# Performance work log

Measured on AMD Instinct MI355X. Metric: run time of the kernel, lower is better.

The kernel has to match this reference:

```python
import jax, jax.numpy as jnp
import numpy as np

D_MODEL = 1024
NUM_HEADS = 16
HEAD_DIM = D_MODEL // NUM_HEADS
THETA = 10000.0
B, S = 4, 2048


def _rope(x, pos):
    # x: [B, H, S, d], pos: [B, S] int
    half = HEAD_DIM // 2
    inv_freq = THETA ** (-(jnp.arange(half, dtype=jnp.float32) * 2.0) / HEAD_DIM)  # [half]
    ang = pos.astype(jnp.float32)[:, None, :, None] * inv_freq  # [B, 1, S, half]
    cos, sin = jnp.cos(ang), jnp.sin(ang)
    x1, x2 = x[..., 0::2], x[..., 1::2]  # interleaved pairs
    r1 = x1 * cos - x2 * sin
    r2 = x1 * sin + x2 * cos
    return jnp.stack([r1, r2], axis=-1).reshape(x.shape)


def setup_inputs() -> dict:
    key = jax.random.key(0)
    ks = jax.random.split(key, 12)
    scale = 1.0 / np.sqrt(D_MODEL)
    inp = {
        "query": jax.random.normal(ks[0], (B, S, D_MODEL), dtype=jnp.float32),
        "key": jax.random.normal(ks[1], (B, S, D_MODEL), dtype=jnp.float32),
        "value": jax.random.normal(ks[2], (B, S, D_MODEL), dtype=jnp.float32),
        "token_positions": jnp.broadcast_to(jnp.arange(S, dtype=jnp.int32), (B, S)),
        "w_q": jax.random.normal(ks[3], (D_MODEL, D_MODEL), dtype=jnp.float32) * scale,
        "b_q": jnp.zeros((D_MODEL,), dtype=jnp.float32),
        "w_k": jax.random.normal(ks[4], (D_MODEL, D_MODEL), dtype=jnp.float32) * scale,
        "b_k": jnp.zeros((D_MODEL,), dtype=jnp.float32),
        "w_v": jax.random.normal(ks[5], (D_MODEL, D_MODEL), dtype=jnp.float32) * scale,
        "b_v": jnp.zeros((D_MODEL,), dtype=jnp.float32),
        "w_o": jax.random.normal(ks[6], (D_MODEL, D_MODEL), dtype=jnp.float32) * scale,
        "b_o": jnp.zeros((D_MODEL,), dtype=jnp.float32),
    }
    return inp


def reference(query, key, value, token_positions, w_q, b_q, w_k, b_k, w_v, b_v, w_o, b_o):
    b, s, _ = query.shape
    Q = query @ w_q + b_q
    K = key @ w_k + b_k
    V = value @ w_v + b_v
    # [B, S, H, d] -> [B, H, S, d]
    Q = Q.reshape(b, s, NUM_HEADS, HEAD_DIM).transpose(0, 2, 1, 3)
    K = K.reshape(b, s, NUM_HEADS, HEAD_DIM).transpose(0, 2, 1, 3)
    V = V.reshape(b, s, NUM_HEADS, HEAD_DIM).transpose(0, 2, 1, 3)
    Q = _rope(Q, token_positions)
    K = _rope(K, token_positions)
    scores = jnp.einsum("bhqd,bhkd->bhqk", Q, K) / jnp.sqrt(jnp.float32(HEAD_DIM))
    causal = jnp.tril(jnp.ones((s, s), dtype=bool))
    scores = jnp.where(causal, scores, -jnp.inf)
    attn = jax.nn.softmax(scores, axis=-1)
    out = jnp.einsum("bhqk,bhkd->bhqd", attn, V)
    out = out.transpose(0, 2, 1, 3).reshape(b, s, D_MODEL)
    return out @ w_o + b_o
```

## Files before the change

### kernel.cpp

```cpp
#include <hip/hip_runtime.h>

typedef __bf16 bf16;
typedef __attribute__((ext_vector_type(8))) __bf16 bf16x8;
typedef __attribute__((ext_vector_type(4))) __bf16 bf16x4;
typedef __attribute__((ext_vector_type(4))) float floatx4;

#define MFMA16(a, b, c) __builtin_amdgcn_mfma_f32_16x16x32_bf16((a), (b), (c), 0, 0, 0)

#define GLL(g, l)                                                   \
  __builtin_amdgcn_global_load_lds(                                 \
      (const __attribute__((address_space(1))) void*)(g),           \
      (__attribute__((address_space(3))) void*)(l), 16, 0, 0)

static constexpr int DM = 1024;
static constexpr int SEQ = 2048;
static constexpr int BATCH = 4;
static constexpr int NH = 16;
static constexpr int HD = 64;
static constexpr float LOG2E = 1.4426950408889634f;
static constexpr float LOG2_THETA = 13.287712379549449f;
static constexpr float QSC = 0.125f * LOG2E;

__global__ __launch_bounds__(256) void prep(
    const float* __restrict__ q, const float* __restrict__ k,
    const float* __restrict__ v, bf16* __restrict__ qo,
    bf16* __restrict__ ko, bf16* __restrict__ vo,
    const float* __restrict__ wq, const float* __restrict__ wk,
    const float* __restrict__ wv, const float* __restrict__ wo,
    bf16* __restrict__ oq, bf16* __restrict__ ok, bf16* __restrict__ ov,
    bf16* __restrict__ oo, const int* __restrict__ tp,
    float* __restrict__ tab) {
  __shared__ __align__(16) bf16 T[64][72];
  int bid = blockIdx.x;
  int tid = threadIdx.x;
  if (bid < 12288) {
    int z = bid >> 12, x = bid & 4095;
    const float* src = (z == 0) ? q : (z == 1) ? k : v;
    bf16* dst = (z == 0) ? qo : (z == 1) ? ko : vo;
    size_t i = ((size_t)x * 256 + tid) * 8;
    float4 a = *(const float4*)(src + i);
    float4 b = *(const float4*)(src + i + 4);
    bf16x8 o;
    o[0] = (bf16)a.x; o[1] = (bf16)a.y; o[2] = (bf16)a.z; o[3] = (bf16)a.w;
    o[4] = (bf16)b.x; o[5] = (bf16)b.y; o[6] = (bf16)b.z; o[7] = (bf16)b.w;
    *(bf16x8*)(dst + i) = o;
  } else if (bid < 13312) {
    int b2 = bid - 12288;
    int z = b2 >> 8, yy = (b2 >> 4) & 15, xx = b2 & 15;
    const float* src = (z == 0) ? wq : (z == 1) ? wk : (z == 2) ? wv : wo;
    bf16* dst = (z == 0) ? oq : (z == 1) ? ok : (z == 2) ? ov : oo;
    int k0 = yy * 64, n0 = xx * 64;
    int r = tid >> 4, c4 = (tid & 15) * 4;
#pragma unroll
    for (int i = 0; i < 4; i++) {
      int kk = r + i * 16;
      float4 vv = *(const float4*)(src + (size_t)(k0 + kk) * DM + n0 + c4);
      T[c4 + 0][kk] = (bf16)vv.x;
      T[c4 + 1][kk] = (bf16)vv.y;
      T[c4 + 2][kk] = (bf16)vv.z;
      T[c4 + 3][kk] = (bf16)vv.w;
    }
    __syncthreads();
#pragma unroll
    for (int i = 0; i < 4; i++) {
      int nn = r + i * 16;
      bf16x4 o = *(const bf16x4*)&T[nn][c4];
      *(bf16x4*)(dst + (size_t)(n0 + nn) * DM + k0 + c4) = o;
    }
  } else {
    int idx = (bid - 13312) * 256 + tid;
    int m = idx >> 5, i = idx & 31;
    float pos = (float)tp[m];
    float invf = exp2f(-(float)(2 * i) * (LOG2_THETA / 64.0f));
    float s, c;
    sincosf(pos * invf, &s, &c);
    tab[(size_t)idx * 2] = c;
    tab[(size_t)idx * 2 + 1] = s;
  }
}

__global__ __launch_bounds__(256) void gemm_qkv(
    const bf16* __restrict__ qb, const bf16* __restrict__ kb,
    const bf16* __restrict__ vb, const bf16* __restrict__ wqt,
    const bf16* __restrict__ wkt, const bf16* __restrict__ wvt,
    const float* __restrict__ biq, const float* __restrict__ bik,
    const float* __restrict__ biv, const float* __restrict__ tab,
    bf16* __restrict__ Qr, bf16* __restrict__ Kr, bf16* __restrict__ Vr) {
  int z = blockIdx.z;
  const bf16* X = (z == 0) ? qb : (z == 1) ? kb : vb;
  const bf16* Wt = (z == 0) ? wqt : (z == 1) ? wkt : wvt;
  const float* bias = (z == 0) ? biq : (z == 1) ? bik : biv;

  __shared__ __align__(16) bf16 As[128 * 64];
  __shared__ __align__(16) bf16 Bs[128 * 64];
  int lin = blockIdx.x;
  int m0 = (lin & 63) * 128, n0 = (lin >> 6) * 128;
  int tid = threadIdx.x;
  int lane = tid & 63, wv = tid >> 6;
  int quad = lane >> 4, low = lane & 15;
  int wm = (wv >> 1) * 64, wn = (wv & 1) * 64;
  int lr8 = lane >> 3;
  int swcol = ((lane & 7) ^ lr8) * 8;
  const bf16* AgL = X + (size_t)(m0 + wv * 8 + lr8) * DM + swcol;
  const bf16* BgL = Wt + (size_t)(n0 + wv * 8 + lr8) * DM + swcol;
  bf16* AsL = As + wv * 8 * 64;
  bf16* BsL = Bs + wv * 8 * 64;
  int r3 = low & 7;

  floatx4 acc[4][4];
#pragma unroll
  for (int i = 0; i < 4; i++)
#pragma unroll
    for (int j = 0; j < 4; j++) acc[i][j] = (floatx4)0.0f;

  for (int kt = 0; kt < DM; kt += 64) {
#pragma unroll
    for (int c = 0; c < 4; c++) {
      GLL(AgL + kt + (size_t)(c * 32) * DM, AsL + c * 2048);
      GLL(BgL + kt + (size_t)(c * 32) * DM, BsL + c * 2048);
    }
    __syncthreads();
#pragma unroll
    for (int kc = 0; kc < 2; kc++) {
      bf16x8 xf[4], wf[4];
#pragma unroll
      for (int t = 0; t < 4; t++)
        xf[t] = *(const bf16x8*)&As[(wm + t * 16 + low) * 64 +
                                    (((kc << 2) | quad) ^ r3) * 8];
#pragma unroll
      for (int t = 0; t < 4; t++)
        wf[t] = *(const bf16x8*)&Bs[(wn + t * 16 + low) * 64 +
                                    (((kc << 2) | quad) ^ r3) * 8];
#pragma unroll
      for (int i = 0; i < 4; i++)
#pragma unroll
        for (int j = 0; j < 4; j++)
          acc[i][j] = MFMA16(wf[i], xf[j], acc[i][j]);
    }
    __syncthreads();
  }

#pragma unroll
  for (int i = 0; i < 4; i++) {
    int nb = n0 + wn + i * 16 + quad * 4;
    float4 bv = *(const float4*)(bias + nb);
    int h = nb >> 6, dbase = nb & 63;
#pragma unroll
    for (int j = 0; j < 4; j++) {
      int m = m0 + wm + j * 16 + low;
      int bb = m >> 11, ss = m & 2047;
      float v0 = acc[i][j][0] + bv.x;
      float v1 = acc[i][j][1] + bv.y;
      float v2 = acc[i][j][2] + bv.z;
      float v3 = acc[i][j][3] + bv.w;
      size_t off = ((size_t)(bb * NH + h) * SEQ + ss) * HD + dbase;
      bf16x4 pk;
      if (z < 2) {
        float4 cs = *(const float4*)(tab + (size_t)m * 64 + dbase);
        float o0 = v0 * cs.x - v1 * cs.y;
        float o1 = v0 * cs.y + v1 * cs.x;
        float o2 = v2 * cs.z - v3 * cs.w;
        float o3 = v2 * cs.w + v3 * cs.z;
        if (z == 0) { o0 *= QSC; o1 *= QSC; o2 *= QSC; o3 *= QSC; }
        pk[0] = (bf16)o0; pk[1] = (bf16)o1;
        pk[2] = (bf16)o2; pk[3] = (bf16)o3;
        bf16* dst = (z == 0) ? Qr : Kr;
        *(bf16x4*)(dst + off) = pk;
      } else {
        pk[0] = (bf16)v0; pk[1] = (bf16)v1;
        pk[2] = (bf16)v2; pk[3] = (bf16)v3;
        *(bf16x4*)(Vr + off) = pk;
      }
    }
  }
}

__global__ __launch_bounds__(256) void transpose_v(const bf16* __restrict__ Vr,
                                                   bf16* __restrict__ Vt) {
  int bh = blockIdx.y;
  int s0 = blockIdx.x * 64;
  __shared__ __align__(16) bf16 T[64][72];
  int t = threadIdx.x;
  int r = t >> 2, c = (t & 3) * 16;
  const bf16* src = Vr + ((size_t)bh * SEQ + s0 + r) * HD + c;
  bf16x8 a = *(const bf16x8*)src;
  bf16x8 b = *(const bf16x8*)(src + 8);
  *(bf16x8*)&T[r][c] = a;
  *(bf16x8*)&T[r][c + 8] = b;
  __syncthreads();
  bf16* dst = Vt + ((size_t)bh * HD + r) * SEQ + s0 + c;
  bf16x8 o0, o1;
#pragma unroll
  for (int j = 0; j < 8; j++) {
    o0[j] = T[c + j][r];
    o1[j] = T[c + 8 + j][r];
  }
  *(bf16x8*)dst = o0;
  *(bf16x8*)(dst + 8) = o1;
}

__global__ __launch_bounds__(256, 3) void attn_fa(const bf16* __restrict__ Qr,
                                                  const bf16* __restrict__ Kr,
                                                  const bf16* __restrict__ Vt,
                                                  bf16* __restrict__ attn) {
  int lin = blockIdx.x;
  int bh = lin & 63, qi = 15 - (lin >> 6);
  int ntiles = 2 * qi + 2;
  int tid = threadIdx.x, lane = tid & 63, w = tid >> 6;
  int quad = lane >> 4, low = lane & 15;
  __shared__ __align__(16) bf16 Ks[2][64 * 72];
  __shared__ __align__(16) bf16 Vs[2][64 * 72];
  const bf16* Qh = Qr + (size_t)bh * SEQ * HD;
  const bf16* Kh = Kr + (size_t)bh * SEQ * HD;
  const bf16* Vh = Vt + (size_t)bh * HD * SEQ;
  int bb = bh >> 4, h = bh & 15;
  int qrow0 = qi * 128 + w * 32;

  int sr = tid >> 2, scol = (tid & 3) * 16;
  const bf16* Kg = Kh + (size_t)sr * HD + scol;
  const bf16* Vg = Vh + (size_t)sr * SEQ + scol;
  int sl = sr * 72 + scol;

  bf16x8 ones;
#pragma unroll
  for (int j = 0; j < 8; j++) ones[j] = (bf16)1.0f;

  bf16x8 aq[2][2];
#pragma unroll
  for (int rt = 0; rt < 2; rt++)
#pragma unroll
    for (int kc = 0; kc < 2; kc++)
      aq[rt][kc] = *(const bf16x8*)(Qh + (size_t)(qrow0 + rt * 16 + low) * HD +
                                    kc * 32 + quad * 8);

  floatx4 accO[2][4];
  floatx4 lacc[2];
#pragma unroll
  for (int rt = 0; rt < 2; rt++) {
    lacc[rt] = (floatx4)0.0f;
#pragma unroll
    for (int nt = 0; nt < 4; nt++) accO[rt][nt] = (floatx4)0.0f;
  }

  {
    bf16x8 k0 = *(const bf16x8*)(Kg);
    bf16x8 k1 = *(const bf16x8*)(Kg + 8);
    bf16x8 v0 = *(const bf16x8*)(Vg);
    bf16x8 v1 = *(const bf16x8*)(Vg + 8);
    *(bf16x8*)&Ks[0][sl] = k0;
    *(bf16x8*)&Ks[0][sl + 8] = k1;
    *(bf16x8*)&Vs[0][sl] = v0;
    *(bf16x8*)&Vs[0][sl + 8] = v1;
  }
  __syncthreads();

  for (int kt = 0; kt < ntiles; kt++) {
    int cur = kt & 1;
    bf16* Pw = &Ks[cur ^ 1][(w * 16) * 72];
    bf16x8 nk0, nk1, nv0, nv1;
    bool pre = (kt + 1 < ntiles);
    if (pre) {
      const bf16* kg = Kg + (size_t)(kt + 1) * (64 * HD);
      const bf16* vg = Vg + (size_t)(kt + 1) * 64;
      nk0 = *(const bf16x8*)(kg);
      nk1 = *(const bf16x8*)(kg + 8);
      nv0 = *(const bf16x8*)(vg);
      nv1 = *(const bf16x8*)(vg + 8);
    }

    floatx4 s2[2][4];
#pragma unroll
    for (int rt = 0; rt < 2; rt++)
#pragma unroll
      for (int nt = 0; nt < 4; nt++) s2[rt][nt] = (floatx4)0.0f;
    __builtin_amdgcn_s_setprio(1);
#pragma unroll
    for (int nt = 0; nt < 4; nt++) {
      bf16x8 kb0 = *(const bf16x8*)&Ks[cur][(nt * 16 + low) * 72 + quad * 8];
      bf16x8 kb1 =
          *(const bf16x8*)&Ks[cur][(nt * 16 + low) * 72 + 32 + quad * 8];
#pragma unroll
      for (int rt = 0; rt < 2; rt++) {
        s2[rt][nt] = MFMA16(kb0, aq[rt][0], s2[rt][nt]);
        s2[rt][nt] = MFMA16(kb1, aq[rt][1], s2[rt][nt]);
      }
    }
    __builtin_amdgcn_s_setprio(0);
    if (kt >= ntiles - 2) {
#pragma unroll
      for (int nt = 0; nt < 4; nt++)
#pragma unroll
        for (int r = 0; r < 4; r++) {
          int kg_ = kt * 64 + nt * 16 + quad * 4 + r;
#pragma unroll
          for (int rt = 0; rt < 2; rt++) {
            int qg = qrow0 + rt * 16 + low;
            if (kg_ > qg) s2[rt][nt][r] = -INFINITY;
          }
        }
    }
    bf16x4 pk[2][4];
#pragma unroll
    for (int rt = 0; rt < 2; rt++)
#pragma unroll
      for (int nt = 0; nt < 4; nt++)
#pragma unroll
        for (int r = 0; r < 4; r++)
          pk[rt][nt][r] = (bf16)exp2f(s2[rt][nt][r]);
    bf16x8 vb0[4], vb1[4];
#pragma unroll
    for (int nt = 0; nt < 4; nt++) {
      vb0[nt] = *(const bf16x8*)&Vs[cur][(nt * 16 + low) * 72 + quad * 8];
      vb1[nt] = *(const bf16x8*)&Vs[cur][(nt * 16 + low) * 72 + 32 + quad * 8];
    }
#pragma unroll
    for (int rt = 0; rt < 2; rt++) {
#pragma unroll
      for (int nt = 0; nt < 4; nt++)
        *(bf16x4*)&Pw[low * 72 + nt * 16 + quad * 4] = pk[rt][nt];
      asm volatile("s_waitcnt lgkmcnt(0)" ::: "memory");
      bf16x8 ap0 = *(const bf16x8*)&Pw[low * 72 + quad * 8];
      bf16x8 ap1 = *(const bf16x8*)&Pw[low * 72 + 32 + quad * 8];
      __builtin_amdgcn_s_setprio(1);
#pragma unroll
      for (int nt = 0; nt < 4; nt++) {
        accO[rt][nt] = MFMA16(ap0, vb0[nt], accO[rt][nt]);
        accO[rt][nt] = MFMA16(ap1, vb1[nt], accO[rt][nt]);
      }
      lacc[rt] = MFMA16(ap0, ones, lacc[rt]);
      lacc[rt] = MFMA16(ap1, ones, lacc[rt]);
      __builtin_amdgcn_s_setprio(0);
    }
    if (pre) {
      int nb = cur ^ 1;
      *(bf16x8*)&Ks[nb][sl] = nk0;
      *(bf16x8*)&Ks[nb][sl + 8] = nk1;
      *(bf16x8*)&Vs[nb][sl] = nv0;
      *(bf16x8*)&Vs[nb][sl + 8] = nv1;
    }
    __syncthreads();
  }

#pragma unroll
  for (int rt = 0; rt < 2; rt++)
#pragma unroll
    for (int r = 0; r < 4; r++) {
      float inv = 1.0f / lacc[rt][r];
      int q = qrow0 + rt * 16 + quad * 4 + r;
#pragma unroll
      for (int nt = 0; nt < 4; nt++) {
        float o = accO[rt][nt][r] * inv;
        attn[((size_t)(bb * SEQ + q)) * DM + h * HD + nt * 16 + low] = (bf16)o;
      }
    }
}

__global__ __launch_bounds__(256) void gemm_out(const bf16* __restrict__ X,
                                                const bf16* __restrict__ Wt,
                                                const float* __restrict__ bias,
                                                float* __restrict__ out) {
  __shared__ __align__(16) bf16 As[128 * 64];
  __shared__ __align__(16) bf16 Bs[128 * 64];
  int lin = blockIdx.x;
  int m0 = (lin & 63) * 128, n0 = (lin >> 6) * 128;
  int tid = threadIdx.x;
  int lane = tid & 63, wv = tid >> 6;
  int quad = lane >> 4, low = lane & 15;
  int wm = (wv >> 1) * 64, wn = (wv & 1) * 64;
  int lr8 = lane >> 3;
  int swcol = ((lane & 7) ^ lr8) * 8;
  const bf16* AgL = X + (size_t)(m0 + wv * 8 + lr8) * DM + swcol;
  const bf16* BgL = Wt + (size_t)(n0 + wv * 8 + lr8) * DM + swcol;
  bf16* AsL = As + wv * 8 * 64;
  bf16* BsL = Bs + wv * 8 * 64;
  int r3 = low & 7;

  floatx4 acc[4][4];
#pragma unroll
  for (int i = 0; i < 4; i++)
#pragma unroll
    for (int j = 0; j < 4; j++) acc[i][j] = (floatx4)0.0f;

  for (int kt = 0; kt < DM; kt += 64) {
#pragma unroll
    for (int c = 0; c < 4; c++) {
      GLL(AgL + kt + (size_t)(c * 32) * DM, AsL + c * 2048);
      GLL(BgL + kt + (size_t)(c * 32) * DM, BsL + c * 2048);
    }
    __syncthreads();
#pragma unroll
    for (int kc = 0; kc < 2; kc++) {
      bf16x8 xf[4], wf[4];
#pragma unroll
      for (int t = 0; t < 4; t++)
        xf[t] = *(const bf16x8*)&As[(wm + t * 16 + low) * 64 +
                                    (((kc << 2) | quad) ^ r3) * 8];
#pragma unroll
      for (int t = 0; t < 4; t++)
        wf[t] = *(const bf16x8*)&Bs[(wn + t * 16 + low) * 64 +
                                    (((kc << 2) | quad) ^ r3) * 8];
#pragma unroll
      for (int i = 0; i < 4; i++)
#pragma unroll
        for (int j = 0; j < 4; j++)
          acc[i][j] = MFMA16(wf[i], xf[j], acc[i][j]);
    }
    __syncthreads();
  }

#pragma unroll
  for (int i = 0; i < 4; i++) {
    int nb = n0 + wn + i * 16 + quad * 4;
    float4 bv = *(const float4*)(bias + nb);
#pragma unroll
    for (int j = 0; j < 4; j++) {
      int m = m0 + wm + j * 16 + low;
      float4 o;
      o.x = acc[i][j][0] + bv.x;
      o.y = acc[i][j][1] + bv.y;
      o.z = acc[i][j][2] + bv.z;
      o.w = acc[i][j][3] + bv.w;
      *(float4*)(out + (size_t)m * DM + nb) = o;
    }
  }
}

extern "C" void kernel_launch(void* const* d_in, const int* in_sizes, int n_in,
                              void* d_out, int out_size, void* d_ws,
                              size_t ws_size, hipStream_t stream) {
  const float* query = (const float*)d_in[0];
  const float* key_ = (const float*)d_in[1];
  const float* value = (const float*)d_in[2];
  const int* tp = (const int*)d_in[3];
  const float* w_q = (const float*)d_in[4];
  const float* b_q = (const float*)d_in[5];
  const float* w_k = (const float*)d_in[6];
  const float* b_k = (const float*)d_in[7];
  const float* w_v = (const float*)d_in[8];
  const float* b_v = (const float*)d_in[9];
  const float* w_o = (const float*)d_in[10];
  const float* b_o = (const float*)d_in[11];

  char* w = (char*)d_ws;
  const size_t MB = 1u << 20;
  bf16* qb = (bf16*)(w + 0);
  bf16* kb = (bf16*)(w + 16 * MB);
  bf16* vb = (bf16*)(w + 32 * MB);
  bf16* wqt = (bf16*)(w + 48 * MB);
  bf16* wkt = (bf16*)(w + 50 * MB);
  bf16* wvt = (bf16*)(w + 52 * MB);
  bf16* wot = (bf16*)(w + 54 * MB);
  bf16* Qr = (bf16*)(w + 56 * MB);
  bf16* Kr = (bf16*)(w + 72 * MB);
  bf16* Vr = (bf16*)(w + 88 * MB);
  float* tab = (float*)(w + 104 * MB);
  bf16* Vt = (bf16*)(w + 32 * MB);
  bf16* attnb = (bf16*)(w + 0);

  prep<<<dim3(14336), 256, 0, stream>>>(query, key_, value, qb, kb, vb, w_q,
                                        w_k, w_v, w_o, wqt, wkt, wvt, wot, tp,
                                        tab);
  gemm_qkv<<<dim3(512, 1, 3), 256, 0, stream>>>(qb, kb, vb, wqt, wkt, wvt,
                                                b_q, b_k, b_v, tab, Qr, Kr,
                                                Vr);
  transpose_v<<<dim3(32, 64), 256, 0, stream>>>(Vr, Vt);
  attn_fa<<<dim3(1024), 256, 0, stream>>>(Qr, Kr, Vt, attnb);
  gemm_out<<<dim3(512), 256, 0, stream>>>(attnb, wot, b_o, (float*)d_out);
}
```

Baseline: 322.5 us.

## Double attention query tile per block and split QKV GEMM into three launches

The attention kernel now gives each block 256 query rows (64 per wave), so each K/V tile loaded into LDS feeds twice as many MFMAs. It adds a dedicated per-wave LDS buffer for P, processes row tiles one at a time to limit live registers, and drops occupancy from 3 to 2 blocks per CU. The block order is changed to pair heavy and light causal tiles. The QKV GEMM is split into three kernel launches with a mode argument instead of one z-indexed grid, which adds launch overhead and removes the overlap between Q, K and V work.

```diff
diff --git a/kernel.cpp b/kernel.cpp
--- a/kernel.cpp
+++ b/kernel.cpp
@@ -80,17 +80,9 @@
 }
 
 __global__ __launch_bounds__(256) void gemm_qkv(
-    const bf16* __restrict__ qb, const bf16* __restrict__ kb,
-    const bf16* __restrict__ vb, const bf16* __restrict__ wqt,
-    const bf16* __restrict__ wkt, const bf16* __restrict__ wvt,
-    const float* __restrict__ biq, const float* __restrict__ bik,
-    const float* __restrict__ biv, const float* __restrict__ tab,
-    bf16* __restrict__ Qr, bf16* __restrict__ Kr, bf16* __restrict__ Vr) {
-  int z = blockIdx.z;
-  const bf16* X = (z == 0) ? qb : (z == 1) ? kb : vb;
-  const bf16* Wt = (z == 0) ? wqt : (z == 1) ? wkt : wvt;
-  const float* bias = (z == 0) ? biq : (z == 1) ? bik : biv;
-
+    const bf16* __restrict__ X, const bf16* __restrict__ Wt,
+    const float* __restrict__ bias, const float* __restrict__ tab,
+    bf16* __restrict__ dstp, int mode) {
   __shared__ __align__(16) bf16 As[128 * 64];
   __shared__ __align__(16) bf16 Bs[128 * 64];
   int lin = blockIdx.x;
@@ -155,22 +147,20 @@
       float v3 = acc[i][j][3] + bv.w;
       size_t off = ((size_t)(bb * NH + h) * SEQ + ss) * HD + dbase;
       bf16x4 pk;
-      if (z < 2) {
+      if (mode < 2) {
         float4 cs = *(const float4*)(tab + (size_t)m * 64 + dbase);
         float o0 = v0 * cs.x - v1 * cs.y;
         float o1 = v0 * cs.y + v1 * cs.x;
         float o2 = v2 * cs.z - v3 * cs.w;
         float o3 = v2 * cs.w + v3 * cs.z;
-        if (z == 0) { o0 *= QSC; o1 *= QSC; o2 *= QSC; o3 *= QSC; }
+        if (mode == 0) { o0 *= QSC; o1 *= QSC; o2 *= QSC; o3 *= QSC; }
         pk[0] = (bf16)o0; pk[1] = (bf16)o1;
         pk[2] = (bf16)o2; pk[3] = (bf16)o3;
-        bf16* dst = (z == 0) ? Qr : Kr;
-        *(bf16x4*)(dst + off) = pk;
       } else {
         pk[0] = (bf16)v0; pk[1] = (bf16)v1;
         pk[2] = (bf16)v2; pk[3] = (bf16)v3;
-        *(bf16x4*)(Vr + off) = pk;
-      }
+      }
+      *(bf16x4*)(dstp + off) = pk;
     }
   }
 }
@@ -199,22 +189,25 @@
   *(bf16x8*)(dst + 8) = o1;
 }
 
-__global__ __launch_bounds__(256, 3) void attn_fa(const bf16* __restrict__ Qr,
+__global__ __launch_bounds__(256, 2) void attn_fa(const bf16* __restrict__ Qr,
                                                   const bf16* __restrict__ Kr,
                                                   const bf16* __restrict__ Vt,
                                                   bf16* __restrict__ attn) {
   int lin = blockIdx.x;
-  int bh = lin & 63, qi = 15 - (lin >> 6);
-  int ntiles = 2 * qi + 2;
+  int bh = lin & 63;
+  int g = lin >> 6;
+  int qi = (g < 4) ? (7 - g) : (g - 4);
+  int ntiles = 4 * qi + 4;
   int tid = threadIdx.x, lane = tid & 63, w = tid >> 6;
   int quad = lane >> 4, low = lane & 15;
   __shared__ __align__(16) bf16 Ks[2][64 * 72];
   __shared__ __align__(16) bf16 Vs[2][64 * 72];
+  __shared__ __align__(16) bf16 Pl[4][16 * 72];
   const bf16* Qh = Qr + (size_t)bh * SEQ * HD;
   const bf16* Kh = Kr + (size_t)bh * SEQ * HD;
   const bf16* Vh = Vt + (size_t)bh * HD * SEQ;
   int bb = bh >> 4, h = bh & 15;
-  int qrow0 = qi * 128 + w * 32;
+  int qrow0 = qi * 256 + w * 64;
 
   int sr = tid >> 2, scol = (tid & 3) * 16;
   const bf16* Kg = Kh + (size_t)sr * HD + scol;
@@ -225,18 +218,18 @@
 #pragma unroll
   for (int j = 0; j < 8; j++) ones[j] = (bf16)1.0f;
 
-  bf16x8 aq[2][2];
-#pragma unroll
-  for (int rt = 0; rt < 2; rt++)
+  bf16x8 aq[4][2];
+#pragma unroll
+  for (int rt = 0; rt < 4; rt++)
 #pragma unroll
     for (int kc = 0; kc < 2; kc++)
       aq[rt][kc] = *(const bf16x8*)(Qh + (size_t)(qrow0 + rt * 16 + low) * HD +
                                     kc * 32 + quad * 8);
 
-  floatx4 accO[2][4];
-  floatx4 lacc[2];
-#pragma unroll
-  for (int rt = 0; rt < 2; rt++) {
+  floatx4 accO[4][4];
+  floatx4 lacc[4];
+#pragma unroll
+  for (int rt = 0; rt < 4; rt++) {
     lacc[rt] = (floatx4)0.0f;
 #pragma unroll
     for (int nt = 0; nt < 4; nt++) accO[rt][nt] = (floatx4)0.0f;
@@ -256,7 +249,7 @@
 
   for (int kt = 0; kt < ntiles; kt++) {
     int cur = kt & 1;
-    bf16* Pw = &Ks[cur ^ 1][(w * 16) * 72];
+    bf16* Pw = &Pl[w][0];
     bf16x8 nk0, nk1, nv0, nv1;
     bool pre = (kt + 1 < ntiles);
     if (pre) {
@@ -268,56 +261,45 @@
       nv1 = *(const bf16x8*)(vg + 8);
     }
 
-    floatx4 s2[2][4];
-#pragma unroll
-    for (int rt = 0; rt < 2; rt++)
-#pragma unroll
-      for (int nt = 0; nt < 4; nt++) s2[rt][nt] = (floatx4)0.0f;
-    __builtin_amdgcn_s_setprio(1);
+    bf16x8 kb0[4], kb1[4], vb0[4], vb1[4];
 #pragma unroll
     for (int nt = 0; nt < 4; nt++) {
-      bf16x8 kb0 = *(const bf16x8*)&Ks[cur][(nt * 16 + low) * 72 + quad * 8];
-      bf16x8 kb1 =
-          *(const bf16x8*)&Ks[cur][(nt * 16 + low) * 72 + 32 + quad * 8];
-#pragma unroll
-      for (int rt = 0; rt < 2; rt++) {
-        s2[rt][nt] = MFMA16(kb0, aq[rt][0], s2[rt][nt]);
-        s2[rt][nt] = MFMA16(kb1, aq[rt][1], s2[rt][nt]);
-      }
-    }
-    __builtin_amdgcn_s_setprio(0);
-    if (kt >= ntiles - 2) {
-#pragma unroll
-      for (int nt = 0; nt < 4; nt++)
-#pragma unroll
-        for (int r = 0; r < 4; r++) {
-          int kg_ = kt * 64 + nt * 16 + quad * 4 + r;
-#pragma unroll
-          for (int rt = 0; rt < 2; rt++) {
-            int qg = qrow0 + rt * 16 + low;
-            if (kg_ > qg) s2[rt][nt][r] = -INFINITY;
-          }
-        }
-    }
-    bf16x4 pk[2][4];
-#pragma unroll
-    for (int rt = 0; rt < 2; rt++)
-#pragma unroll
-      for (int nt = 0; nt < 4; nt++)
-#pragma unroll
-        for (int r = 0; r < 4; r++)
-          pk[rt][nt][r] = (bf16)exp2f(s2[rt][nt][r]);
-    bf16x8 vb0[4], vb1[4];
-#pragma unroll
-    for (int nt = 0; nt < 4; nt++) {
+      kb0[nt] = *(const bf16x8*)&Ks[cur][(nt * 16 + low) * 72 + quad * 8];
+      kb1[nt] = *(const bf16x8*)&Ks[cur][(nt * 16 + low) * 72 + 32 + quad * 8];
       vb0[nt] = *(const bf16x8*)&Vs[cur][(nt * 16 + low) * 72 + quad * 8];
       vb1[nt] = *(const bf16x8*)&Vs[cur][(nt * 16 + low) * 72 + 32 + quad * 8];
     }
-#pragma unroll
-    for (int rt = 0; rt < 2; rt++) {
+
+#pragma unroll
+    for (int rt = 0; rt < 4; rt++) {
+      floatx4 s2[4];
+#pragma unroll
+      for (int nt = 0; nt < 4; nt++) s2[nt] = (floatx4)0.0f;
+      __builtin_amdgcn_s_setprio(1);
+#pragma unroll
+      for (int nt = 0; nt < 4; nt++) {
+        s2[nt] = MFMA16(kb0[nt], aq[rt][0], s2[nt]);
+        s2[nt] = MFMA16(kb1[nt], aq[rt][1], s2[nt]);
+      }
+      __builtin_amdgcn_s_setprio(0);
+      if (kt >= ntiles - 4) {
+#pragma unroll
+        for (int nt = 0; nt < 4; nt++)
+#pragma unroll
+          for (int r = 0; r < 4; r++) {
+            int kg_ = kt * 64 + nt * 16 + quad * 4 + r;
+            int qg = qrow0 + rt * 16 + low;
+            if (kg_ > qg) s2[nt][r] = -INFINITY;
+          }
+      }
+      bf16x4 pk[4];
 #pragma unroll
       for (int nt = 0; nt < 4; nt++)
-        *(bf16x4*)&Pw[low * 72 + nt * 16 + quad * 4] = pk[rt][nt];
+#pragma unroll
+        for (int r = 0; r < 4; r++) pk[nt][r] = (bf16)exp2f(s2[nt][r]);
+#pragma unroll
+      for (int nt = 0; nt < 4; nt++)
+        *(bf16x4*)&Pw[low * 72 + nt * 16 + quad * 4] = pk[nt];
       asm volatile("s_waitcnt lgkmcnt(0)" ::: "memory");
       bf16x8 ap0 = *(const bf16x8*)&Pw[low * 72 + quad * 8];
       bf16x8 ap1 = *(const bf16x8*)&Pw[low * 72 + 32 + quad * 8];
@@ -330,19 +312,19 @@
       lacc[rt] = MFMA16(ap0, ones, lacc[rt]);
       lacc[rt] = MFMA16(ap1, ones, lacc[rt]);
       __builtin_amdgcn_s_setprio(0);
-    }
-    if (pre) {
-      int nb = cur ^ 1;
-      *(bf16x8*)&Ks[nb][sl] = nk0;
-      *(bf16x8*)&Ks[nb][sl + 8] = nk1;
-      *(bf16x8*)&Vs[nb][sl] = nv0;
-      *(bf16x8*)&Vs[nb][sl + 8] = nv1;
-    }
-    __syncthreads();
-  }
-
-#pragma unroll
-  for (int rt = 0; rt < 2; rt++)
+      if (rt == 1 && pre) {
+        int nb = cur ^ 1;
+        *(bf16x8*)&Ks[nb][sl] = nk0;
+        *(bf16x8*)&Ks[nb][sl + 8] = nk1;
+        *(bf16x8*)&Vs[nb][sl] = nv0;
+        *(bf16x8*)&Vs[nb][sl + 8] = nv1;
+      }
+    }
+    __syncthreads();
+  }
+
+#pragma unroll
+  for (int rt = 0; rt < 4; rt++)
 #pragma unroll
     for (int r = 0; r < 4; r++) {
       float inv = 1.0f / lacc[rt][r];
@@ -460,10 +442,10 @@
   prep<<<dim3(14336), 256, 0, stream>>>(query, key_, value, qb, kb, vb, w_q,
                                         w_k, w_v, w_o, wqt, wkt, wvt, wot, tp,
                                         tab);
-  gemm_qkv<<<dim3(512, 1, 3), 256, 0, stream>>>(qb, kb, vb, wqt, wkt, wvt,
-                                                b_q, b_k, b_v, tab, Qr, Kr,
-                                                Vr);
+  gemm_qkv<<<dim3(512), 256, 0, stream>>>(qb, wqt, b_q, tab, Qr, 0);
+  gemm_qkv<<<dim3(512), 256, 0, stream>>>(kb, wkt, b_k, tab, Kr, 1);
+  gemm_qkv<<<dim3(512), 256, 0, stream>>>(vb, wvt, b_v, tab, Vr, 2);
   transpose_v<<<dim3(32, 64), 256, 0, stream>>>(Vr, Vt);
-  attn_fa<<<dim3(1024), 256, 0, stream>>>(Qr, Kr, Vt, attnb);
+  attn_fa<<<dim3(512), 256, 0, stream>>>(Qr, Kr, Vt, attnb);
   gemm_out<<<dim3(512), 256, 0, stream>>>(attnb, wot, b_o, (float*)d_out);
 }
```

Result: slower. 346.7 us (+7.5%).
